# Kernel optimization log

Measured on AMD Instinct MI355X. Metric: run time of the kernel, lower is better.

## Reference

```python
import jax, jax.numpy as jnp
import numpy as np

EMB = 2048
NH = 16
HD = EMB // NH  # 128

def setup_inputs() -> dict:
    key = jax.random.key(0)
    kx, kw1, kw2 = jax.random.split(key, 3)
    T = 4096
    x = jax.random.normal(kx, (T, EMB), dtype=jnp.float32)
    lim_in = 1.0 / np.sqrt(EMB)
    # input_proj: Linear(EMB, 3*EMB, use_bias=False), weight shape (out, in)
    W_in = jax.random.uniform(kw1, (3 * EMB, EMB), minval=-lim_in, maxval=lim_in, dtype=jnp.float32)
    W_out = jax.random.uniform(kw2, (EMB, EMB), minval=-lim_in, maxval=lim_in, dtype=jnp.float32)
    return {"x": x, "W_in": W_in, "W_out": W_out}

def reference(x, W_in, W_out):
    T = x.shape[0]
    norm = 1.0 / np.sqrt(HD)
    qkv = x @ W_in.T                         # [T, 3E]
    Q, K, V = jnp.split(qkv, 3, axis=-1)     # each [T, E]
    Q = Q.reshape(T, NH, HD).transpose(1, 0, 2)  # [nh, T, hd]
    K = K.reshape(T, NH, HD).transpose(1, 0, 2)
    V = V.reshape(T, NH, HD).transpose(1, 0, 2)
    A = jnp.einsum('htd,hsd->hts', Q, K) * norm  # [nh, T, T]
    mask = jnp.tri(T, dtype=bool)                # causal: keep lower triangle
    A = jnp.where(mask, A, -jnp.inf)
    P = jax.nn.softmax(A, axis=-1)
    y = jnp.einsum('hts,hsd->htd', P, V)         # [nh, T, hd]
    y = y.transpose(1, 0, 2).reshape(T, EMB)     # concat heads
    return y @ W_out.T
```

## Files before the change

kernel.cpp:

```cpp
#include <hip/hip_runtime.h>
#include <hip/hip_bf16.h>
#include <cstddef>


typedef __attribute__((ext_vector_type(8))) short short8;
typedef __attribute__((ext_vector_type(4))) float f32x4;

#define MFMA16(a, b, c) __builtin_amdgcn_mfma_f32_16x16x32_bf16((a), (b), (c), 0, 0, 0)

#define GLOAD_LDS16(gptr, lptr)                                                          \
  __builtin_amdgcn_global_load_lds((const __attribute__((address_space(1))) void*)(gptr), \
                                   (__attribute__((address_space(3))) void*)(lptr), 16, 0, 0)

#define VSWZ(f) ((((f) & 7) ^ (((f) >> 3) & 7)) << 3)

__device__ __forceinline__ short f2bf(float f) {
  __hip_bfloat16 h = __float2bfloat16(f);
  return *reinterpret_cast<short*>(&h);
}

__device__ __forceinline__ void storeC(float* p, float v) { *p = v; }
__device__ __forceinline__ void storeC(short* p, float v) { *p = f2bf(v); }

__global__ void cvt_bf16(const float* __restrict__ in, short* __restrict__ out, long n) {
  long i = ((long)blockIdx.x * 256 + threadIdx.x) * 8;
  if (i >= n) return;
  f32x4 a = *(const f32x4*)(in + i);
  f32x4 b = *(const f32x4*)(in + i + 4);
  short8 o;
  o[0] = f2bf(a[0]); o[1] = f2bf(a[1]); o[2] = f2bf(a[2]); o[3] = f2bf(a[3]);
  o[4] = f2bf(b[0]); o[5] = f2bf(b[1]); o[6] = f2bf(b[2]); o[7] = f2bf(b[3]);
  *(short8*)(out + i) = o;
}

template <typename CT>
__global__ __launch_bounds__(256, 2)
void gemm_bt(const short* __restrict__ A, const short* __restrict__ B,
             CT* __restrict__ C, int M, int N, int K, float cscale, int nscale) {
  __shared__ short As[128 * 32];
  __shared__ short Bs[128 * 32];
  const int tid = threadIdx.x;
  const int wave = tid >> 6, lane = tid & 63;
  const int g = lane >> 4, fr = lane & 15;
  const int wr = (wave >> 1) * 64, wc = (wave & 1) * 64;
  const int bm = blockIdx.y * 128, bn = blockIdx.x * 128;

  f32x4 acc[4][4] = {};

  for (int k0 = 0; k0 < K; k0 += 32) {
    __syncthreads();
#pragma unroll
    for (int i = 0; i < 2; ++i) {
      int Ci = i * 256 + tid;
      int row = Ci >> 2, c = Ci & 3;
      int sc = c ^ (row & 3);
      GLOAD_LDS16(A + (size_t)(bm + row) * K + k0 + sc * 8, As + Ci * 8);
      GLOAD_LDS16(B + (size_t)(bn + row) * K + k0 + sc * 8, Bs + Ci * 8);
    }
    __syncthreads();

    short8 af[4], bfr[4];
#pragma unroll
    for (int m = 0; m < 4; ++m) {
      int row = wr + m * 16 + fr;
      int off = (g * 8) ^ ((row & 3) * 8);
      af[m] = *(const short8*)(As + row * 32 + off);
    }
#pragma unroll
    for (int n = 0; n < 4; ++n) {
      int row = wc + n * 16 + fr;
      int off = (g * 8) ^ ((row & 3) * 8);
      bfr[n] = *(const short8*)(Bs + row * 32 + off);
    }
#pragma unroll
    for (int m = 0; m < 4; ++m)
#pragma unroll
      for (int n = 0; n < 4; ++n)
        acc[m][n] = MFMA16(af[m], bfr[n], acc[m][n]);
  }

#pragma unroll
  for (int m = 0; m < 4; ++m) {
#pragma unroll
    for (int r = 0; r < 4; ++r) {
      size_t row = (size_t)(bm + wr + m * 16 + g * 4 + r);
      CT* cp = C + row * N + bn + wc + fr;
#pragma unroll
      for (int n = 0; n < 4; ++n) {
        float sc = (bn + wc + n * 16 + fr < nscale) ? cscale : 1.0f;
        storeC(cp + n * 16, acc[m][n][r] * sc);
      }
    }
  }
}

__global__ __launch_bounds__(256, 2)
void attn_fwd(const short* __restrict__ qkv, short* __restrict__ y) {
  __shared__ short Ks[2][64 * 128];
  __shared__ short Vt[128 * 64];
  __shared__ short Ps[4 * 16 * 72];
  const int tid = threadIdx.x;
  const int wave = tid >> 6, lane = tid & 63;
  const int g = lane >> 4, fr = lane & 15;

  const int wgid = blockIdx.x;
  const int slot = wgid >> 3;
  const int h = ((wgid & 7) << 1) | (slot >> 5);
  const int pair = slot & 31;

  short* Pw = Ps + wave * (16 * 72);

  short8 onesf;
#pragma unroll
  for (int j = 0; j < 8; ++j) onesf[j] = (short)0x3F80;

#pragma unroll 1
  for (int phase = 0; phase < 2; ++phase) {
    const int xb = phase ? (63 - pair) : pair;
    const int qw = xb * 64 + wave * 16;
    const int ntiles = xb + 1;

    short8 qf[4];
    {
      const short* Qp = qkv + (size_t)(qw + fr) * 6144 + h * 128;
#pragma unroll
      for (int kk = 0; kk < 4; ++kk)
        qf[kk] = *(const short8*)(Qp + kk * 32 + g * 8);
    }
    f32x4 oacc[8] = {};
    f32x4 lacc = {};

#pragma unroll
    for (int i = 0; i < 4; ++i) {
      int Ci = i * 256 + tid, key = Ci >> 4, c = Ci & 15, sc = c ^ (key & 7);
      GLOAD_LDS16(qkv + (size_t)key * 6144 + 2048 + h * 128 + sc * 8, &Ks[0][Ci * 8]);
    }
    __syncthreads();

#pragma unroll 1
    for (int t = 0; t < ntiles; ++t) {
      const int kv0 = t * 64;
      const int cur = t & 1;

      if (t + 1 < ntiles) {
#pragma unroll
        for (int i = 0; i < 4; ++i) {
          int Ci = i * 256 + tid, key = Ci >> 4, c = Ci & 15, sc = c ^ (key & 7);
          GLOAD_LDS16(qkv + (size_t)(kv0 + 64 + key) * 6144 + 2048 + h * 128 + sc * 8,
                      &Ks[cur ^ 1][Ci * 8]);
        }
      }
      short8 vreg[4];
#pragma unroll
      for (int i = 0; i < 4; ++i) {
        int Ci = i * 256 + tid, key = Ci >> 4, c = Ci & 15;
        vreg[i] = *(const short8*)(qkv + (size_t)(kv0 + key) * 6144 + 4096 + h * 128 + c * 8);
      }

      f32x4 s[4] = {};
      __builtin_amdgcn_s_setprio(1);
#pragma unroll
      for (int nf = 0; nf < 4; ++nf) {
        const int key = nf * 16 + fr;
#pragma unroll
        for (int kk = 0; kk < 4; ++kk) {
          int off = (kk * 32 + g * 8) ^ ((key & 7) * 8);
          short8 kfrag = *(const short8*)(&Ks[cur][key * 128 + off]);
          s[nf] = MFMA16(qf[kk], kfrag, s[nf]);
        }
      }
      __builtin_amdgcn_s_setprio(0);

      if (t == ntiles - 1) {
#pragma unroll
        for (int nf = 0; nf < 4; ++nf) {
          const int keyg = kv0 + nf * 16 + fr;
#pragma unroll
          for (int r = 0; r < 4; ++r) {
            const int q = g * 4 + r;
            float p = (keyg <= qw + q) ? __builtin_amdgcn_exp2f(s[nf][r]) : 0.f;
            Pw[q * 72 + ((nf * 16 + fr) ^ ((q >> 3) << 3))] = f2bf(p);
          }
        }
      } else {
#pragma unroll
        for (int nf = 0; nf < 4; ++nf)
#pragma unroll
          for (int r = 0; r < 4; ++r) {
            const int q = g * 4 + r;
            Pw[q * 72 + ((nf * 16 + fr) ^ ((q >> 3) << 3))] =
                f2bf(__builtin_amdgcn_exp2f(s[nf][r]));
          }
      }

      __syncthreads();

#pragma unroll
      for (int i = 0; i < 4; ++i) {
        int Ci = i * 256 + tid, key = Ci >> 4, c = Ci & 15;
#pragma unroll
        for (int j = 0; j < 8; ++j) {
          int f = c * 8 + j;
          Vt[f * 64 + (key ^ VSWZ(f))] = vreg[i][j];
        }
      }
      __syncthreads();

      __builtin_amdgcn_s_setprio(1);
#pragma unroll
      for (int kk = 0; kk < 2; ++kk) {
        short8 pf = *(const short8*)(&Pw[fr * 72 + ((kk * 32 + g * 8) ^ ((fr >> 3) << 3))]);
        lacc = MFMA16(pf, onesf, lacc);
#pragma unroll
        for (int nf = 0; nf < 8; ++nf) {
          int f = nf * 16 + fr;
          short8 vf = *(const short8*)(&Vt[f * 64 + ((kk * 32 + g * 8) ^ VSWZ(f))]);
          oacc[nf] = MFMA16(pf, vf, oacc[nf]);
        }
      }
      __builtin_amdgcn_s_setprio(0);
    }

#pragma unroll
    for (int r = 0; r < 4; ++r) {
      float inv = 1.0f / lacc[r];
      size_t row = (size_t)(qw + g * 4 + r);
#pragma unroll
      for (int nf = 0; nf < 8; ++nf)
        y[row * 2048 + h * 128 + nf * 16 + fr] = f2bf(oacc[nf][r] * inv);
    }
  }
}

extern "C" void kernel_launch(void* const* d_in, const int* in_sizes, int n_in,
                              void* d_out, int out_size, void* d_ws, size_t ws_size,
                              hipStream_t stream) {
  const float* x    = (const float*)d_in[0];
  const float* Win  = (const float*)d_in[1];
  const float* Wout = (const float*)d_in[2];
  float* out = (float*)d_out;

  char* ws = (char*)d_ws;
  short* xb    = (short*)(ws);
  short* Winb  = (short*)(ws + 16777216);
  short* Woutb = (short*)(ws + 41943040);
  short* qkv   = (short*)(ws + 50331648);
  short* yb    = (short*)(ws + 100663296);

  cvt_bf16<<<4096, 256, 0, stream>>>(x, xb, 8388608L);
  cvt_bf16<<<6144, 256, 0, stream>>>(Win, Winb, 12582912L);
  cvt_bf16<<<2048, 256, 0, stream>>>(Wout, Woutb, 4194304L);

  const float qscale = 0.08838834764831845f * 1.4426950408889634f;
  gemm_bt<short><<<dim3(48, 32), 256, 0, stream>>>(xb, Winb, qkv, 4096, 6144, 2048,
                                                   qscale, 2048);

  attn_fwd<<<512, 256, 0, stream>>>(qkv, yb);

  gemm_bt<float><<<dim3(16, 32), 256, 0, stream>>>(yb, Woutb, out, 4096, 2048, 2048,
                                                   1.0f, 0);
}
```

Before: 329.2 us.

## Emit V pre-transposed from QKV GEMM and double-buffer V tiles via async LDS loads

The QKV projection epilogue now writes V in a transposed, pre-swizzled global layout, with Q and K kept in a narrower buffer. The attention kernel therefore loads V tiles straight into LDS with async global-to-LDS copies, double-buffered like K. This drops the per-tile register transpose into LDS and one of the two barriers per tile. The cost is scattered 2-byte stores in the GEMM epilogue for the V columns, which may be poorly coalesced, plus more LDS per block.

```diff
diff --git a/kernel.cpp b/kernel.cpp
--- a/kernel.cpp
+++ b/kernel.cpp
@@ -11,8 +11,6 @@
 #define GLOAD_LDS16(gptr, lptr)                                                          \
   __builtin_amdgcn_global_load_lds((const __attribute__((address_space(1))) void*)(gptr), \
                                    (__attribute__((address_space(3))) void*)(lptr), 16, 0, 0)
-
-#define VSWZ(f) ((((f) & 7) ^ (((f) >> 3) & 7)) << 3)
 
 __device__ __forceinline__ short f2bf(float f) {
   __hip_bfloat16 h = __float2bfloat16(f);
@@ -33,10 +31,11 @@
   *(short8*)(out + i) = o;
 }
 
-template <typename CT>
+template <typename CT, bool VT>
 __global__ __launch_bounds__(256, 2)
 void gemm_bt(const short* __restrict__ A, const short* __restrict__ B,
-             CT* __restrict__ C, int M, int N, int K, float cscale, int nscale) {
+             CT* __restrict__ C, short* __restrict__ vtg,
+             int M, int N, int K, int ldc, float cscale, int nscale) {
   __shared__ short As[128 * 32];
   __shared__ short Bs[128 * 32];
   const int tid = threadIdx.x;
@@ -79,26 +78,36 @@
         acc[m][n] = MFMA16(af[m], bfr[n], acc[m][n]);
   }
 
+  const bool isv = VT && (bn + wc) >= 4096;
 #pragma unroll
   for (int m = 0; m < 4; ++m) {
 #pragma unroll
     for (int r = 0; r < 4; ++r) {
-      size_t row = (size_t)(bm + wr + m * 16 + g * 4 + r);
-      CT* cp = C + row * N + bn + wc + fr;
+      int row = bm + wr + m * 16 + g * 4 + r;
 #pragma unroll
       for (int n = 0; n < 4; ++n) {
-        float sc = (bn + wc + n * 16 + fr < nscale) ? cscale : 1.0f;
-        storeC(cp + n * 16, acc[m][n][r] * sc);
+        int col = bn + wc + n * 16 + fr;
+        float val = acc[m][n][r] * ((col < nscale) ? cscale : 1.0f);
+        if (isv) {
+          int hf = col - 4096;
+          int feat = hf & 127;
+          size_t addr = (size_t)hf * 4096 +
+                        (size_t)((row & ~63) | ((row & 63) ^ ((feat & 7) << 3)));
+          vtg[addr] = f2bf(val);
+        } else {
+          storeC(C + (size_t)row * ldc + col, val);
+        }
       }
     }
   }
 }
 
 __global__ __launch_bounds__(256, 2)
-void attn_fwd(const short* __restrict__ qkv, short* __restrict__ y) {
+void attn_fwd(const short* __restrict__ qk, const short* __restrict__ vtg,
+              short* __restrict__ y) {
   __shared__ short Ks[2][64 * 128];
-  __shared__ short Vt[128 * 64];
-  __shared__ short Ps[4 * 16 * 72];
+  __shared__ short Vt[2][128 * 64];
+  __shared__ short Ps[4][16 * 72];
   const int tid = threadIdx.x;
   const int wave = tid >> 6, lane = tid & 63;
   const int g = lane >> 4, fr = lane & 15;
@@ -108,7 +117,7 @@
   const int h = ((wgid & 7) << 1) | (slot >> 5);
   const int pair = slot & 31;
 
-  short* Pw = Ps + wave * (16 * 72);
+  short* Pw = Ps[wave];
 
   short8 onesf;
 #pragma unroll
@@ -122,7 +131,7 @@
 
     short8 qf[4];
     {
-      const short* Qp = qkv + (size_t)(qw + fr) * 6144 + h * 128;
+      const short* Qp = qk + (size_t)(qw + fr) * 4096 + h * 128;
 #pragma unroll
       for (int kk = 0; kk < 4; ++kk)
         qf[kk] = *(const short8*)(Qp + kk * 32 + g * 8);
@@ -133,7 +142,12 @@
 #pragma unroll
     for (int i = 0; i < 4; ++i) {
       int Ci = i * 256 + tid, key = Ci >> 4, c = Ci & 15, sc = c ^ (key & 7);
-      GLOAD_LDS16(qkv + (size_t)key * 6144 + 2048 + h * 128 + sc * 8, &Ks[0][Ci * 8]);
+      GLOAD_LDS16(qk + (size_t)key * 4096 + 2048 + h * 128 + sc * 8, &Ks[0][Ci * 8]);
+    }
+#pragma unroll
+    for (int i = 0; i < 4; ++i) {
+      int Ci = i * 256 + tid, feat = Ci >> 3, ko = (Ci & 7) * 8;
+      GLOAD_LDS16(vtg + (size_t)(h * 128 + feat) * 4096 + ko, &Vt[0][Ci * 8]);
     }
     __syncthreads();
 
@@ -146,15 +160,15 @@
 #pragma unroll
         for (int i = 0; i < 4; ++i) {
           int Ci = i * 256 + tid, key = Ci >> 4, c = Ci & 15, sc = c ^ (key & 7);
-          GLOAD_LDS16(qkv + (size_t)(kv0 + 64 + key) * 6144 + 2048 + h * 128 + sc * 8,
+          GLOAD_LDS16(qk + (size_t)(kv0 + 64 + key) * 4096 + 2048 + h * 128 + sc * 8,
                       &Ks[cur ^ 1][Ci * 8]);
         }
-      }
-      short8 vreg[4];
-#pragma unroll
-      for (int i = 0; i < 4; ++i) {
-        int Ci = i * 256 + tid, key = Ci >> 4, c = Ci & 15;
-        vreg[i] = *(const short8*)(qkv + (size_t)(kv0 + key) * 6144 + 4096 + h * 128 + c * 8);
+#pragma unroll
+        for (int i = 0; i < 4; ++i) {
+          int Ci = i * 256 + tid, feat = Ci >> 3, ko = (Ci & 7) * 8;
+          GLOAD_LDS16(vtg + (size_t)(h * 128 + feat) * 4096 + kv0 + 64 + ko,
+                      &Vt[cur ^ 1][Ci * 8]);
+        }
       }
 
       f32x4 s[4] = {};
@@ -193,19 +207,6 @@
           }
       }
 
-      __syncthreads();
-
-#pragma unroll
-      for (int i = 0; i < 4; ++i) {
-        int Ci = i * 256 + tid, key = Ci >> 4, c = Ci & 15;
-#pragma unroll
-        for (int j = 0; j < 8; ++j) {
-          int f = c * 8 + j;
-          Vt[f * 64 + (key ^ VSWZ(f))] = vreg[i][j];
-        }
-      }
-      __syncthreads();
-
       __builtin_amdgcn_s_setprio(1);
 #pragma unroll
       for (int kk = 0; kk < 2; ++kk) {
@@ -214,11 +215,13 @@
 #pragma unroll
         for (int nf = 0; nf < 8; ++nf) {
           int f = nf * 16 + fr;
-          short8 vf = *(const short8*)(&Vt[f * 64 + ((kk * 32 + g * 8) ^ VSWZ(f))]);
+          short8 vf = *(const short8*)(&Vt[cur][f * 64 + ((kk * 32 + g * 8) ^ ((f & 7) * 8))]);
           oacc[nf] = MFMA16(pf, vf, oacc[nf]);
         }
       }
       __builtin_amdgcn_s_setprio(0);
+
+      __syncthreads();
     }
 
 #pragma unroll
@@ -244,7 +247,8 @@
   short* xb    = (short*)(ws);
   short* Winb  = (short*)(ws + 16777216);
   short* Woutb = (short*)(ws + 41943040);
-  short* qkv   = (short*)(ws + 50331648);
+  short* qk    = (short*)(ws + 50331648);
+  short* vtg   = (short*)(ws + 83886080);
   short* yb    = (short*)(ws + 100663296);
 
   cvt_bf16<<<4096, 256, 0, stream>>>(x, xb, 8388608L);
@@ -252,11 +256,11 @@
   cvt_bf16<<<2048, 256, 0, stream>>>(Wout, Woutb, 4194304L);
 
   const float qscale = 0.08838834764831845f * 1.4426950408889634f;
-  gemm_bt<short><<<dim3(48, 32), 256, 0, stream>>>(xb, Winb, qkv, 4096, 6144, 2048,
-                                                   qscale, 2048);
-
-  attn_fwd<<<512, 256, 0, stream>>>(qkv, yb);
-
-  gemm_bt<float><<<dim3(16, 32), 256, 0, stream>>>(yb, Woutb, out, 4096, 2048, 2048,
-                                                   1.0f, 0);
-}
+  gemm_bt<short, true><<<dim3(48, 32), 256, 0, stream>>>(
+      xb, Winb, qk, vtg, 4096, 6144, 2048, 4096, qscale, 2048);
+
+  attn_fwd<<<512, 256, 0, stream>>>(qk, vtg, yb);
+
+  gemm_bt<float, false><<<dim3(16, 32), 256, 0, stream>>>(
+      yb, Woutb, out, nullptr, 4096, 2048, 2048, 2048, 1.0f, 0);
+}
```

Result: faster. 311.7 us (-5.3%).

## Pre-transpose V globally and double per-wave query rows in attention

Applied to the files above, without the earlier changes.

Adds a separate kernel that writes V transposed per head into workspace, so the attention kernel can stream V tiles straight into LDS with async loads and double buffering. This removes the per-tile register-to-LDS scatter and one barrier. Each wave now handles 32 query rows instead of 16, so every K/V fragment read from LDS is reused twice. The grid is halved to 256 blocks with one block per CU as the launch bound, which risks lower occupancy and load imbalance. The workspace is reused by aliasing buffers, and there is an extra kernel launch plus extra global traffic for the transpose.

```diff
diff --git a/kernel.cpp b/kernel.cpp
--- a/kernel.cpp
+++ b/kernel.cpp
@@ -11,8 +11,6 @@
 #define GLOAD_LDS16(gptr, lptr)                                                          \
   __builtin_amdgcn_global_load_lds((const __attribute__((address_space(1))) void*)(gptr), \
                                    (__attribute__((address_space(3))) void*)(lptr), 16, 0, 0)
-
-#define VSWZ(f) ((((f) & 7) ^ (((f) >> 3) & 7)) << 3)
 
 __device__ __forceinline__ short f2bf(float f) {
   __hip_bfloat16 h = __float2bfloat16(f);
@@ -94,21 +92,50 @@
   }
 }
 
-__global__ __launch_bounds__(256, 2)
-void attn_fwd(const short* __restrict__ qkv, short* __restrict__ y) {
+__global__ __launch_bounds__(256, 4)
+void vtrans(const short* __restrict__ qkv, short* __restrict__ vtg) {
+  __shared__ short L[128 * 64];
+  const int tid = threadIdx.x;
+  const int tb = blockIdx.x * 64;
+  const int h = blockIdx.y;
+#pragma unroll
+  for (int i = 0; i < 4; ++i) {
+    int Ci = i * 256 + tid, tok = Ci >> 4, c = Ci & 15, f0 = c * 8;
+    short8 v = *(const short8*)(qkv + (size_t)(tb + tok) * 6144 + 4096 + h * 128 + f0);
+#pragma unroll
+    for (int j = 0; j < 8; ++j) {
+      int f = f0 + j;
+      L[f * 64 + (tok ^ ((((f & 7) ^ ((f >> 3) & 7)) << 3)))] = v[j];
+    }
+  }
+  __syncthreads();
+  const int f = tid >> 1, half = (tid & 1) * 32;
+  const int s_in = ((f & 7) ^ ((f >> 3) & 7)) << 3;
+  const int s_out = (f & 7) << 3;
+#pragma unroll
+  for (int j2 = 0; j2 < 4; ++j2) {
+    int t0 = half + j2 * 8;
+    short8 v = *(const short8*)(&L[f * 64 + (t0 ^ s_in)]);
+    *(short8*)(vtg + (size_t)(h * 128 + f) * 4096 + tb + (t0 ^ s_out)) = v;
+  }
+}
+
+__global__ __launch_bounds__(256, 1)
+void attn_fwd(const short* __restrict__ qkv, const short* __restrict__ vtg,
+              short* __restrict__ y) {
   __shared__ short Ks[2][64 * 128];
-  __shared__ short Vt[128 * 64];
-  __shared__ short Ps[4 * 16 * 72];
+  __shared__ short Vt[2][128 * 64];
+  __shared__ short Ps[4][32 * 72];
   const int tid = threadIdx.x;
   const int wave = tid >> 6, lane = tid & 63;
   const int g = lane >> 4, fr = lane & 15;
 
   const int wgid = blockIdx.x;
   const int slot = wgid >> 3;
-  const int h = ((wgid & 7) << 1) | (slot >> 5);
-  const int pair = slot & 31;
-
-  short* Pw = Ps + wave * (16 * 72);
+  const int h = ((wgid & 7) << 1) | (slot >> 4);
+  const int pair = slot & 15;
+
+  short* Pw = Ps[wave];
 
   short8 onesf;
 #pragma unroll
@@ -116,24 +143,30 @@
 
 #pragma unroll 1
   for (int phase = 0; phase < 2; ++phase) {
-    const int xb = phase ? (63 - pair) : pair;
-    const int qw = xb * 64 + wave * 16;
-    const int ntiles = xb + 1;
-
-    short8 qf[4];
-    {
-      const short* Qp = qkv + (size_t)(qw + fr) * 6144 + h * 128;
+    const int xb = phase ? (31 - pair) : pair;
+    const int qw = xb * 128 + wave * 32;
+    const int ntiles = 2 * xb + 2;
+
+    short8 qf[2][4];
+#pragma unroll
+    for (int mi = 0; mi < 2; ++mi) {
+      const short* Qp = qkv + (size_t)(qw + mi * 16 + fr) * 6144 + h * 128;
 #pragma unroll
       for (int kk = 0; kk < 4; ++kk)
-        qf[kk] = *(const short8*)(Qp + kk * 32 + g * 8);
-    }
-    f32x4 oacc[8] = {};
-    f32x4 lacc = {};
+        qf[mi][kk] = *(const short8*)(Qp + kk * 32 + g * 8);
+    }
+    f32x4 oacc[2][8] = {};
+    f32x4 lacc[2] = {};
 
 #pragma unroll
     for (int i = 0; i < 4; ++i) {
       int Ci = i * 256 + tid, key = Ci >> 4, c = Ci & 15, sc = c ^ (key & 7);
       GLOAD_LDS16(qkv + (size_t)key * 6144 + 2048 + h * 128 + sc * 8, &Ks[0][Ci * 8]);
+    }
+#pragma unroll
+    for (int i = 0; i < 4; ++i) {
+      int Ci = i * 256 + tid, feat = Ci >> 3, ko = (Ci & 7) * 8;
+      GLOAD_LDS16(vtg + (size_t)(h * 128 + feat) * 4096 + ko, &Vt[0][Ci * 8]);
     }
     __syncthreads();
 
@@ -149,15 +182,15 @@
           GLOAD_LDS16(qkv + (size_t)(kv0 + 64 + key) * 6144 + 2048 + h * 128 + sc * 8,
                       &Ks[cur ^ 1][Ci * 8]);
         }
-      }
-      short8 vreg[4];
-#pragma unroll
-      for (int i = 0; i < 4; ++i) {
-        int Ci = i * 256 + tid, key = Ci >> 4, c = Ci & 15;
-        vreg[i] = *(const short8*)(qkv + (size_t)(kv0 + key) * 6144 + 4096 + h * 128 + c * 8);
-      }
-
-      f32x4 s[4] = {};
+#pragma unroll
+        for (int i = 0; i < 4; ++i) {
+          int Ci = i * 256 + tid, feat = Ci >> 3, ko = (Ci & 7) * 8;
+          GLOAD_LDS16(vtg + (size_t)(h * 128 + feat) * 4096 + kv0 + 64 + ko,
+                      &Vt[cur ^ 1][Ci * 8]);
+        }
+      }
+
+      f32x4 s[2][4] = {};
       __builtin_amdgcn_s_setprio(1);
 #pragma unroll
       for (int nf = 0; nf < 4; ++nf) {
@@ -166,69 +199,69 @@
         for (int kk = 0; kk < 4; ++kk) {
           int off = (kk * 32 + g * 8) ^ ((key & 7) * 8);
           short8 kfrag = *(const short8*)(&Ks[cur][key * 128 + off]);
-          s[nf] = MFMA16(qf[kk], kfrag, s[nf]);
+          s[0][nf] = MFMA16(qf[0][kk], kfrag, s[0][nf]);
+          s[1][nf] = MFMA16(qf[1][kk], kfrag, s[1][nf]);
         }
       }
       __builtin_amdgcn_s_setprio(0);
 
-      if (t == ntiles - 1) {
-#pragma unroll
-        for (int nf = 0; nf < 4; ++nf) {
-          const int keyg = kv0 + nf * 16 + fr;
-#pragma unroll
-          for (int r = 0; r < 4; ++r) {
-            const int q = g * 4 + r;
-            float p = (keyg <= qw + q) ? __builtin_amdgcn_exp2f(s[nf][r]) : 0.f;
-            Pw[q * 72 + ((nf * 16 + fr) ^ ((q >> 3) << 3))] = f2bf(p);
+      if (t >= ntiles - 2) {
+#pragma unroll
+        for (int mi = 0; mi < 2; ++mi)
+#pragma unroll
+          for (int nf = 0; nf < 4; ++nf) {
+            const int keyg = kv0 + nf * 16 + fr;
+#pragma unroll
+            for (int r = 0; r < 4; ++r) {
+              const int q2 = mi * 16 + g * 4 + r;
+              float p = (keyg <= qw + q2) ? __builtin_amdgcn_exp2f(s[mi][nf][r]) : 0.f;
+              Pw[q2 * 72 + ((nf * 16 + fr) ^ (((q2 >> 3) & 3) << 3))] = f2bf(p);
+            }
           }
-        }
       } else {
 #pragma unroll
-        for (int nf = 0; nf < 4; ++nf)
-#pragma unroll
-          for (int r = 0; r < 4; ++r) {
-            const int q = g * 4 + r;
-            Pw[q * 72 + ((nf * 16 + fr) ^ ((q >> 3) << 3))] =
-                f2bf(__builtin_amdgcn_exp2f(s[nf][r]));
-          }
-      }
-
-      __syncthreads();
-
-#pragma unroll
-      for (int i = 0; i < 4; ++i) {
-        int Ci = i * 256 + tid, key = Ci >> 4, c = Ci & 15;
-#pragma unroll
-        for (int j = 0; j < 8; ++j) {
-          int f = c * 8 + j;
-          Vt[f * 64 + (key ^ VSWZ(f))] = vreg[i][j];
-        }
-      }
-      __syncthreads();
+        for (int mi = 0; mi < 2; ++mi)
+#pragma unroll
+          for (int nf = 0; nf < 4; ++nf)
+#pragma unroll
+            for (int r = 0; r < 4; ++r) {
+              const int q2 = mi * 16 + g * 4 + r;
+              Pw[q2 * 72 + ((nf * 16 + fr) ^ (((q2 >> 3) & 3) << 3))] =
+                  f2bf(__builtin_amdgcn_exp2f(s[mi][nf][r]));
+            }
+      }
 
       __builtin_amdgcn_s_setprio(1);
 #pragma unroll
       for (int kk = 0; kk < 2; ++kk) {
-        short8 pf = *(const short8*)(&Pw[fr * 72 + ((kk * 32 + g * 8) ^ ((fr >> 3) << 3))]);
-        lacc = MFMA16(pf, onesf, lacc);
+        const int rb = kk * 32 + g * 8;
+        short8 pf0 = *(const short8*)(&Pw[fr * 72 + (rb ^ ((fr >> 3) << 3))]);
+        short8 pf1 = *(const short8*)(&Pw[(16 + fr) * 72 + (rb ^ ((2 + (fr >> 3)) << 3))]);
+        lacc[0] = MFMA16(pf0, onesf, lacc[0]);
+        lacc[1] = MFMA16(pf1, onesf, lacc[1]);
 #pragma unroll
         for (int nf = 0; nf < 8; ++nf) {
           int f = nf * 16 + fr;
-          short8 vf = *(const short8*)(&Vt[f * 64 + ((kk * 32 + g * 8) ^ VSWZ(f))]);
-          oacc[nf] = MFMA16(pf, vf, oacc[nf]);
+          short8 vf = *(const short8*)(&Vt[cur][f * 64 + (rb ^ ((f & 7) * 8))]);
+          oacc[0][nf] = MFMA16(pf0, vf, oacc[0][nf]);
+          oacc[1][nf] = MFMA16(pf1, vf, oacc[1][nf]);
         }
       }
       __builtin_amdgcn_s_setprio(0);
-    }
-
-#pragma unroll
-    for (int r = 0; r < 4; ++r) {
-      float inv = 1.0f / lacc[r];
-      size_t row = (size_t)(qw + g * 4 + r);
-#pragma unroll
-      for (int nf = 0; nf < 8; ++nf)
-        y[row * 2048 + h * 128 + nf * 16 + fr] = f2bf(oacc[nf][r] * inv);
-    }
+
+      __syncthreads();
+    }
+
+#pragma unroll
+    for (int mi = 0; mi < 2; ++mi)
+#pragma unroll
+      for (int r = 0; r < 4; ++r) {
+        float inv = 1.0f / lacc[mi][r];
+        size_t row = (size_t)(qw + mi * 16 + g * 4 + r);
+#pragma unroll
+        for (int nf = 0; nf < 8; ++nf)
+          y[row * 2048 + h * 128 + nf * 16 + fr] = f2bf(oacc[mi][nf][r] * inv);
+      }
   }
 }
 
@@ -242,10 +275,11 @@
 
   char* ws = (char*)d_ws;
   short* xb    = (short*)(ws);
+  short* yb    = (short*)(ws);
   short* Winb  = (short*)(ws + 16777216);
+  short* vtg   = (short*)(ws + 16777216);
   short* Woutb = (short*)(ws + 41943040);
   short* qkv   = (short*)(ws + 50331648);
-  short* yb    = (short*)(ws + 100663296);
 
   cvt_bf16<<<4096, 256, 0, stream>>>(x, xb, 8388608L);
   cvt_bf16<<<6144, 256, 0, stream>>>(Win, Winb, 12582912L);
@@ -255,7 +289,9 @@
   gemm_bt<short><<<dim3(48, 32), 256, 0, stream>>>(xb, Winb, qkv, 4096, 6144, 2048,
                                                    qscale, 2048);
 
-  attn_fwd<<<512, 256, 0, stream>>>(qkv, yb);
+  vtrans<<<dim3(64, 16), 256, 0, stream>>>(qkv, vtg);
+
+  attn_fwd<<<256, 256, 0, stream>>>(qkv, vtg, yb);
 
   gemm_bt<float><<<dim3(16, 32), 256, 0, stream>>>(yb, Woutb, out, 4096, 2048, 2048,
                                                    1.0f, 0);
```

Result: no change. 333.2 us (+1.2%).
